# Optimization experiments

Hardware: AMD Instinct MI355X
Metric: run time of the kernel (lower is better)

The kernel has to match this reference:

```python
import jax, jax.numpy as jnp
import numpy as np

WIN = 5          # ssim_window_size
SIGMA = 1.5      # Gaussian sigma used by the reference implementation
C1 = 0.01 ** 2
C2 = 0.03 ** 2
MS_WEIGHTS = jnp.array([0.0448, 0.2856, 0.3001, 0.2363, 0.1333], dtype=jnp.float32)


def make_window(num_channel, dtype):
    x = jnp.arange(WIN, dtype=jnp.float32) - (WIN // 2)
    g = jnp.exp(-(x ** 2) / (2.0 * SIGMA ** 2))
    g = g / g.sum()
    w2 = jnp.outer(g, g)
    return jnp.broadcast_to(w2, (num_channel, 1, WIN, WIN)).astype(dtype)


def dwconv(x, w):
    pad = WIN // 2
    return jax.lax.conv_general_dilated(
        x, w, window_strides=(1, 1), padding=[(pad, pad), (pad, pad)],
        dimension_numbers=('NCHW', 'OIHW', 'NCHW'),
        feature_group_count=x.shape[1])


def compute_ssim(img1, img2):
    w = make_window(img1.shape[1], img1.dtype)
    mu1 = dwconv(img1, w)
    mu2 = dwconv(img2, w)
    mu1_sq = mu1 * mu1
    mu2_sq = mu2 * mu2
    mu1_mu2 = mu1 * mu2
    sigma1_sq = dwconv(img1 * img1, w) - mu1_sq
    sigma2_sq = dwconv(img2 * img2, w) - mu2_sq
    sigma12 = dwconv(img1 * img2, w) - mu1_mu2
    ssim_map = ((2 * mu1_mu2 + C1) * (2 * sigma12 + C2)) / (
        (mu1_sq + mu2_sq + C1) * (sigma1_sq + sigma2_sq + C2))
    cs = jnp.mean((2.0 * sigma12 + C2) / (sigma1_sq + sigma2_sq + C2))
    return jnp.mean(ssim_map), cs


def avg_pool2(x):
    s = jax.lax.reduce_window(x, jnp.array(0, x.dtype), jax.lax.add,
                              (1, 1, 2, 2), (1, 1, 2, 2), 'VALID')
    return s / jnp.array(4, x.dtype)


def ms_ssim(img1, img2):
    levels = MS_WEIGHTS.shape[0]
    ssims, mcs = [], []
    for _ in range(levels):
        s, cs = compute_ssim(img1, img2)
        ssims.append(s)
        mcs.append(cs)
        img1 = avg_pool2(img1)
        img2 = avg_pool2(img2)
    ssims = (jnp.stack(ssims) + 1) / 2
    mcs = (jnp.stack(mcs) + 1) / 2
    pow1 = mcs ** MS_WEIGHTS
    pow2 = ssims ** MS_WEIGHTS
    return jnp.prod(pow1[:-1] * pow2[-1])


def setup_inputs() -> dict:
    key = jax.random.key(0)
    k1, k2 = jax.random.split(key)
    shape = (32, 3, 512, 512)
    img1 = jax.random.uniform(k1, shape, dtype=jnp.float32)
    img2 = jax.random.uniform(k2, shape, dtype=jnp.float32)
    return {"img1": img1, "img2": img2}


def reference(img1, img2):
    return ms_ssim(img1, img2)
```

## Files before the change

### kernel.cpp

```cpp
#include <hip/hip_runtime.h>
#include <math.h>


typedef float f2 __attribute__((ext_vector_type(2)));

#if __has_builtin(__builtin_elementwise_fma)
static __device__ __forceinline__ f2 vfma(f2 a, f2 b, f2 c) {
    return __builtin_elementwise_fma(a, b, c);
}
#else
static __device__ __forceinline__ f2 vfma(f2 a, f2 b, f2 c) {
    f2 d; d.x = __builtin_fmaf(a.x, b.x, c.x); d.y = __builtin_fmaf(a.y, b.y, c.y);
    return d;
}
#endif

#define C1F 0.0001f
#define C2F 0.0009f
#define GW0f 0.12007838f
#define GW1f 0.23388060f
#define GW2f 0.29208204f

#define HCONV(DST, VL, V01, VR) do { \
    const f2 t1_ = (VL) + (VR); \
    f2 mid_; mid_.x = (VL).y + (V01).y; mid_.y = (V01).x + (VR).x; \
    (DST) = vfma(G1v, mid_, vfma(G0v, t1_, G2v * (V01))); \
} while (0)

#define VCONV(OUT, WN, S0,S1,S2,S3,S4) do { \
    const f2 t_ = WN[S0] + WN[S4]; \
    const f2 u_ = WN[S1] + WN[S3]; \
    (OUT) = vfma(G1v, u_, vfma(G0v, t_, G2v * WN[S2])); \
} while (0)

#define ROW(J,S0,S1,S2,S3,S4) do { \
    const int i = i0 + (J); \
    if (i < iters) { \
        const int r = y0 + i - 2; \
        f2 XL = {0.f,0.f}, X01 = {0.f,0.f}, XR = {0.f,0.f}; \
        f2 ZL = {0.f,0.f}, Z01 = {0.f,0.f}, ZR = {0.f,0.f}; \
        if ((unsigned)r < (unsigned)H) { \
            const float* r1_ = p1 + (size_t)r * (size_t)W; \
            const float* r2_ = p2 + (size_t)r * (size_t)W; \
            XL  = *(const f2*)(r1_ + offL) * mL; \
            X01 = *(const f2*)(r1_ + offC); \
            XR  = *(const f2*)(r1_ + offR) * mR; \
            ZL  = *(const f2*)(r2_ + offL) * mL; \
            Z01 = *(const f2*)(r2_ + offC); \
            ZR  = *(const f2*)(r2_ + offR) * mR; \
        } \
        const f2 QL = vfma(ZL,  ZL,  XL  * XL); \
        const f2 QC = vfma(Z01, Z01, X01 * X01); \
        const f2 QR = vfma(ZR,  ZR,  XR  * XR); \
        const f2 PL = XL  * ZL; \
        const f2 PC = X01 * Z01; \
        const f2 PR = XR  * ZR; \
        HCONV(wa[(J)], XL, X01, XR); \
        HCONV(wb[(J)], ZL, Z01, ZR); \
        HCONV(wq[(J)], QL, QC,  QR); \
        HCONV(wp[(J)], PL, PC,  PR); \
        if (i >= 4) { \
            f2 Av, Bv, Qv, Pv; \
            VCONV(Av, wa, S0,S1,S2,S3,S4); \
            VCONV(Bv, wb, S0,S1,S2,S3,S4); \
            VCONV(Qv, wq, S0,S1,S2,S3,S4); \
            VCONV(Pv, wp, S0,S1,S2,S3,S4); \
            const f2 ABv   = Av * Bv; \
            const f2 A2B2v = vfma(Bv, Bv, Av * Av); \
            const f2 S12v  = vfma(TWOv, Pv - ABv, C2v); \
            const f2 SDENv = (Qv - A2B2v) + C2v; \
            const f2 D1v   = A2B2v + C1v; \
            const f2 N1v   = vfma(TWOv, ABv, C1v); \
            const f2 DENv  = D1v * SDENv; \
            f2 RDv; \
            RDv.x = __builtin_amdgcn_rcpf(DENv.x); \
            RDv.y = __builtin_amdgcn_rcpf(DENv.y); \
            const f2 SSv = N1v * S12v * RDv; \
            const f2 CCv = S12v * D1v * RDv; \
            if (gC) { ACCS += SSv; ACCC += CCv; } \
        } \
        if (q1 && (i & 1) && i >= 3 && i <= TROWS + 1 && gC) { \
            const f2 sx_ = X01 + PX; \
            const f2 sz_ = Z01 + PZ; \
            const size_t po_ = (size_t)(r >> 1) * WP + (c0 >> 1); \
            q1[po_] = (sx_.x + sx_.y) * 0.25f; \
            q2[po_] = (sz_.x + sz_.y) * 0.25f; \
        } \
        PX = X01; PZ = Z01; \
    } \
} while (0)

template<int TROWS, int WPB>
__global__ __launch_bounds__(WPB * 64)
void ssim_level_kernel(const float* __restrict__ img1,
                       const float* __restrict__ img2,
                       int H, int W, int SX, int SY,
                       float* __restrict__ pool1,
                       float* __restrict__ pool2,
                       double* __restrict__ block_out)
{
    const int lane = threadIdx.x & 63;
    const int wv   = threadIdx.x >> 6;
    const int w    = blockIdx.x * WPB + wv;

    const int spp   = SX * SY;
    const int plane = w / spp;
    const int rem   = w - plane * spp;
    const int sy    = rem / SX;
    const int sx    = rem - sy * SX;

    const int base = sx * 128;
    const int y0   = sy * TROWS;
    const int c0   = base + 2 * lane;
    const bool gC = (unsigned)c0 < (unsigned)W;
    const bool gL = (c0 - 2) >= 0 && (c0 - 2) < W;
    const bool gR = (c0 + 2) < W;
    const int offL = gL ? (c0 - 2) : c0;
    const int offC = gC ? c0 : 0;
    const int offR = gR ? (c0 + 2) : 0;
    const f2 mL = {gL ? 1.f : 0.f, gL ? 1.f : 0.f};
    const f2 mR = {gR ? 1.f : 0.f, gR ? 1.f : 0.f};

    const float* p1 = img1 + (size_t)plane * H * W;
    const float* p2 = img2 + (size_t)plane * H * W;
    const int WP = W >> 1;
    float* q1 = pool1 ? pool1 + (size_t)plane * (H >> 1) * WP : nullptr;
    float* q2 = pool2 ? pool2 + (size_t)plane * (H >> 1) * WP : nullptr;

    const f2 G0v  = {GW0f, GW0f};
    const f2 G1v  = {GW1f, GW1f};
    const f2 G2v  = {GW2f, GW2f};
    const f2 C1v  = {C1F, C1F};
    const f2 C2v  = {C2F, C2F};
    const f2 TWOv = {2.f, 2.f};

    f2 wa[5], wb[5], wq[5], wp[5];
    f2 PX = {0.f, 0.f}, PZ = {0.f, 0.f};
    f2 ACCS = {0.f, 0.f}, ACCC = {0.f, 0.f};

    const int iters = TROWS + 4;
    for (int i0 = 0; i0 < iters; i0 += 5) {
        ROW(0, 1, 2, 3, 4, 0);
        ROW(1, 2, 3, 4, 0, 1);
        ROW(2, 3, 4, 0, 1, 2);
        ROW(3, 4, 0, 1, 2, 3);
        ROW(4, 0, 1, 2, 3, 4);
    }

    float accs = ACCS.x + ACCS.y;
    float accc = ACCC.x + ACCC.y;
    #pragma unroll
    for (int o = 32; o > 0; o >>= 1) {
        accs += __shfl_down(accs, o, 64);
        accc += __shfl_down(accc, o, 64);
    }

    __shared__ double sred[WPB][2];
    if (lane == 0) { sred[wv][0] = (double)accs; sred[wv][1] = (double)accc; }
    __syncthreads();
    if (threadIdx.x == 0) {
        double s = 0.0, c = 0.0;
        #pragma unroll
        for (int k = 0; k < WPB; ++k) { s += sred[k][0]; c += sred[k][1]; }
        block_out[2 * (size_t)blockIdx.x]     = s;
        block_out[2 * (size_t)blockIdx.x + 1] = c;
    }
}

static constexpr int NBLK[5] = {1536, 768, 384, 384, 192};
static constexpr int BOFF[5] = {0, 1536, 2304, 2688, 3072};

__global__ __launch_bounds__(1024)
void ssim_final_kernel(const double* __restrict__ bsum, float* __restrict__ out)
{
    __shared__ double partial[16][2];
    __shared__ double lvl[5][2];
    const double npx[5] = {96.0*512*512, 96.0*256*256, 96.0*128*128,
                           96.0*64*64,   96.0*32*32};
    const int tid = threadIdx.x, lane = tid & 63, wv = tid >> 6;

    for (int l = 0; l < 5; ++l) {
        double s = 0.0, c = 0.0;
        for (int k = tid; k < NBLK[l]; k += 1024) {
            s += bsum[2 * (size_t)(BOFF[l] + k)];
            c += bsum[2 * (size_t)(BOFF[l] + k) + 1];
        }
        #pragma unroll
        for (int o = 32; o > 0; o >>= 1) {
            s += __shfl_down(s, o, 64);
            c += __shfl_down(c, o, 64);
        }
        if (lane == 0) { partial[wv][0] = s; partial[wv][1] = c; }
        __syncthreads();
        if (tid == 0) {
            double ts = 0.0, tc = 0.0;
            for (int k = 0; k < 16; ++k) { ts += partial[k][0]; tc += partial[k][1]; }
            lvl[l][0] = ts / npx[l];
            lvl[l][1] = tc / npx[l];
        }
        __syncthreads();
    }
    if (tid == 0) {
        const double wgt[5] = {0.0448, 0.2856, 0.3001, 0.2363, 0.1333};
        double ssim4 = (lvl[4][0] + 1.0) * 0.5;
        double P = pow(ssim4, wgt[4]);
        double r = pow((lvl[0][1] + 1.0) * 0.5, wgt[0]) *
                   pow((lvl[1][1] + 1.0) * 0.5, wgt[1]) *
                   pow((lvl[2][1] + 1.0) * 0.5, wgt[2]) *
                   pow((lvl[3][1] + 1.0) * 0.5, wgt[3]);
        r *= P * P * P * P;
        out[0] = (float)r;
    }
}

extern "C" void kernel_launch(void* const* d_in, const int* in_sizes, int n_in,
                              void* d_out, int out_size, void* d_ws, size_t ws_size,
                              hipStream_t stream)
{
    const float* img1 = (const float*)d_in[0];
    const float* img2 = (const float*)d_in[1];
    float* out = (float*)d_out;

    char* ws = (char*)d_ws;
    double* wsum = (double*)ws;
    size_t off = 262144;
    const size_t P = 96;
    float* l1a = (float*)(ws + off); off += P * 256 * 256 * sizeof(float);
    float* l1b = (float*)(ws + off); off += P * 256 * 256 * sizeof(float);
    float* l2a = (float*)(ws + off); off += P * 128 * 128 * sizeof(float);
    float* l2b = (float*)(ws + off); off += P * 128 * 128 * sizeof(float);
    float* l3a = (float*)(ws + off); off += P * 64 * 64 * sizeof(float);
    float* l3b = (float*)(ws + off); off += P * 64 * 64 * sizeof(float);
    float* l4a = (float*)(ws + off); off += P * 32 * 32 * sizeof(float);
    float* l4b = (float*)(ws + off); off += P * 32 * 32 * sizeof(float);

    ssim_level_kernel<32, 4><<<1536, 256, 0, stream>>>(
        img1, img2, 512, 512, 4, 16, l1a, l1b, wsum + 2 * (size_t)BOFF[0]);
    ssim_level_kernel<16, 4><<<768, 256, 0, stream>>>(
        l1a, l1b, 256, 256, 2, 16, l2a, l2b, wsum + 2 * (size_t)BOFF[1]);
    ssim_level_kernel<8, 4><<<384, 256, 0, stream>>>(
        l2a, l2b, 128, 128, 1, 16, l3a, l3b, wsum + 2 * (size_t)BOFF[2]);
    ssim_level_kernel<4, 4><<<384, 256, 0, stream>>>(
        l3a, l3b, 64, 64, 1, 16, l4a, l4b, wsum + 2 * (size_t)BOFF[3]);
    ssim_level_kernel<4, 4><<<192, 256, 0, stream>>>(
        l4a, l4b, 32, 32, 1, 8, nullptr, nullptr, wsum + 2 * (size_t)BOFF[4]);

    ssim_final_kernel<<<1, 1024, 0, stream>>>(wsum, out);
}
```

Measured before the change: 300.8 us.

## Stage SSIM rows through LDS with async global_load_lds double buffering

Each level kernel now uses one wave per block that loads five-row batches of both images directly into LDS with global_load_lds, double-buffered with explicit vmcnt waits, then reads neighbors from LDS instead of issuing overlapping global loads. Column tiles overlap by halo (124 output columns per 128 loaded), tile heights and grids are retuned per level, and sizes are made compile-time template parameters. The per-block shared-memory reduction is dropped since each block is a single wave, at the cost of many more partial sums for the final kernel and redundant halo loads.

```diff
diff --git a/kernel.cpp b/kernel.cpp
--- a/kernel.cpp
+++ b/kernel.cpp
@@ -14,6 +14,18 @@
     return d;
 }
 #endif
+
+typedef __attribute__((address_space(1))) void gv_t;
+typedef __attribute__((address_space(3))) void lv_t;
+
+static __device__ __forceinline__ void gl_lds(const float* g, float* l) {
+    __builtin_amdgcn_global_load_lds((gv_t*)g, (lv_t*)l, 4, 0, 0);
+}
+
+#define WAITVM(N) do { \
+    asm volatile("s_waitcnt vmcnt(" #N ")" ::: "memory"); \
+    __builtin_amdgcn_sched_barrier(0); \
+} while (0)
 
 #define C1F 0.0001f
 #define C2F 0.0009f
@@ -33,97 +45,130 @@
     (OUT) = vfma(G1v, u_, vfma(G0v, t_, G2v * WN[S2])); \
 } while (0)
 
-#define ROW(J,S0,S1,S2,S3,S4) do { \
-    const int i = i0 + (J); \
-    if (i < iters) { \
-        const int r = y0 + i - 2; \
-        f2 XL = {0.f,0.f}, X01 = {0.f,0.f}, XR = {0.f,0.f}; \
-        f2 ZL = {0.f,0.f}, Z01 = {0.f,0.f}, ZR = {0.f,0.f}; \
-        if ((unsigned)r < (unsigned)H) { \
-            const float* r1_ = p1 + (size_t)r * (size_t)W; \
-            const float* r2_ = p2 + (size_t)r * (size_t)W; \
-            XL  = *(const f2*)(r1_ + offL) * mL; \
-            X01 = *(const f2*)(r1_ + offC); \
-            XR  = *(const f2*)(r1_ + offR) * mR; \
-            ZL  = *(const f2*)(r2_ + offL) * mL; \
-            Z01 = *(const f2*)(r2_ + offC); \
-            ZR  = *(const f2*)(r2_ + offR) * mR; \
-        } \
-        const f2 QL = vfma(ZL,  ZL,  XL  * XL); \
-        const f2 QC = vfma(Z01, Z01, X01 * X01); \
-        const f2 QR = vfma(ZR,  ZR,  XR  * XR); \
-        const f2 PL = XL  * ZL; \
-        const f2 PC = X01 * Z01; \
-        const f2 PR = XR  * ZR; \
-        HCONV(wa[(J)], XL, X01, XR); \
-        HCONV(wb[(J)], ZL, Z01, ZR); \
-        HCONV(wq[(J)], QL, QC,  QR); \
-        HCONV(wp[(J)], PL, PC,  PR); \
-        if (i >= 4) { \
-            f2 Av, Bv, Qv, Pv; \
-            VCONV(Av, wa, S0,S1,S2,S3,S4); \
-            VCONV(Bv, wb, S0,S1,S2,S3,S4); \
-            VCONV(Qv, wq, S0,S1,S2,S3,S4); \
-            VCONV(Pv, wp, S0,S1,S2,S3,S4); \
-            const f2 ABv   = Av * Bv; \
-            const f2 A2B2v = vfma(Bv, Bv, Av * Av); \
-            const f2 S12v  = vfma(TWOv, Pv - ABv, C2v); \
-            const f2 SDENv = (Qv - A2B2v) + C2v; \
-            const f2 D1v   = A2B2v + C1v; \
-            const f2 N1v   = vfma(TWOv, ABv, C1v); \
-            const f2 DENv  = D1v * SDENv; \
-            f2 RDv; \
-            RDv.x = __builtin_amdgcn_rcpf(DENv.x); \
-            RDv.y = __builtin_amdgcn_rcpf(DENv.y); \
-            const f2 SSv = N1v * S12v * RDv; \
-            const f2 CCv = S12v * D1v * RDv; \
-            if (gC) { ACCS += SSv; ACCC += CCv; } \
-        } \
-        if (q1 && (i & 1) && i >= 3 && i <= TROWS + 1 && gC) { \
+#define LOADB(T, B) do { \
+    _Pragma("unroll") \
+    for (int k_ = 0; k_ < 5; ++k_) { \
+        const int r_ = y0 + (T) * 5 + k_ - 2; \
+        const int rc_ = min(max(r_, 0), H - 1); \
+        const float* r1_ = p1 + (size_t)rc_ * W; \
+        const float* r2_ = p2 + (size_t)rc_ * W; \
+        gl_lds(r1_ + col1, &lds[B][k_][0][2]); \
+        gl_lds(r1_ + col2, &lds[B][k_][0][66]); \
+        gl_lds(r2_ + col1, &lds[B][k_][1][2]); \
+        gl_lds(r2_ + col2, &lds[B][k_][1][66]); \
+    } \
+} while (0)
+
+#define STEP(I, K, B, S0,S1,S2,S3,S4) do { \
+    const int r = y0 + (I) - 2; \
+    const float rv = ((unsigned)r < (unsigned)H) ? 1.f : 0.f; \
+    const f2 mVv = {rv, rv}; \
+    const f2 mLVv = mLv * mVv; \
+    const f2 mCVv = mCv * mVv; \
+    const f2 mRVv = mRv * mVv; \
+    const f2 XL  = *(const f2*)&lds[B][K][0][2 * lane]     * mLVv; \
+    const f2 X01 = *(const f2*)&lds[B][K][0][2 * lane + 2] * mCVv; \
+    const f2 XR  = *(const f2*)&lds[B][K][0][2 * lane + 4] * mRVv; \
+    const f2 ZL  = *(const f2*)&lds[B][K][1][2 * lane]     * mLVv; \
+    const f2 Z01 = *(const f2*)&lds[B][K][1][2 * lane + 2] * mCVv; \
+    const f2 ZR  = *(const f2*)&lds[B][K][1][2 * lane + 4] * mRVv; \
+    const f2 QL = vfma(ZL,  ZL,  XL  * XL); \
+    const f2 QC = vfma(Z01, Z01, X01 * X01); \
+    const f2 QR = vfma(ZR,  ZR,  XR  * XR); \
+    const f2 PL = XL  * ZL; \
+    const f2 PC = X01 * Z01; \
+    const f2 PR = XR  * ZR; \
+    HCONV(wa[(S4)], XL, X01, XR); \
+    HCONV(wb[(S4)], ZL, Z01, ZR); \
+    HCONV(wq[(S4)], QL, QC,  QR); \
+    HCONV(wp[(S4)], PL, PC,  PR); \
+    if ((I) >= 4) { \
+        f2 Av, Bv, Qv, Pv; \
+        VCONV(Av, wa, S0,S1,S2,S3,S4); \
+        VCONV(Bv, wb, S0,S1,S2,S3,S4); \
+        VCONV(Qv, wq, S0,S1,S2,S3,S4); \
+        VCONV(Pv, wp, S0,S1,S2,S3,S4); \
+        const f2 ABv   = Av * Bv; \
+        const f2 A2B2v = vfma(Bv, Bv, Av * Av); \
+        const f2 S12v  = vfma(TWOv, Pv - ABv, C2v); \
+        const f2 SDENv = (Qv - A2B2v) + C2v; \
+        const f2 D1v   = A2B2v + C1v; \
+        const f2 N1v   = vfma(TWOv, ABv, C1v); \
+        const f2 DENv  = D1v * SDENv; \
+        f2 RDv; \
+        RDv.x = __builtin_amdgcn_rcpf(DENv.x); \
+        RDv.y = __builtin_amdgcn_rcpf(DENv.y); \
+        const f2 SSv = N1v * S12v * RDv; \
+        const f2 CCv = S12v * D1v * RDv; \
+        ACCS += vout ? SSv : ZEROv; \
+        ACCC += vout ? CCv : ZEROv; \
+    } \
+    { \
+        const bool pcond = (TROWS == 1) ? ((I) == 2 && (y0 & 1)) \
+                          : (((I) & 1) && (I) >= 3 && (I) <= TROWS + 1); \
+        if (q1 && pcond && vout) { \
             const f2 sx_ = X01 + PX; \
             const f2 sz_ = Z01 + PZ; \
             const size_t po_ = (size_t)(r >> 1) * WP + (c0 >> 1); \
             q1[po_] = (sx_.x + sx_.y) * 0.25f; \
             q2[po_] = (sz_.x + sz_.y) * 0.25f; \
         } \
-        PX = X01; PZ = Z01; \
     } \
-} while (0)
-
-template<int TROWS, int WPB>
-__global__ __launch_bounds__(WPB * 64)
+    PX = X01; PZ = Z01; \
+} while (0)
+
+#define BATCH(T, B) do { \
+    STEP((T)*5+0, 0, B, 1,2,3,4,0); \
+    STEP((T)*5+1, 1, B, 2,3,4,0,1); \
+    STEP((T)*5+2, 2, B, 3,4,0,1,2); \
+    STEP((T)*5+3, 3, B, 4,0,1,2,3); \
+    STEP((T)*5+4, 4, B, 0,1,2,3,4); \
+} while (0)
+
+template<int TROWS, int H, int W, int SX>
+__global__ __launch_bounds__(64)
 void ssim_level_kernel(const float* __restrict__ img1,
                        const float* __restrict__ img2,
-                       int H, int W, int SX, int SY,
                        float* __restrict__ pool1,
                        float* __restrict__ pool2,
                        double* __restrict__ block_out)
 {
-    const int lane = threadIdx.x & 63;
-    const int wv   = threadIdx.x >> 6;
-    const int w    = blockIdx.x * WPB + wv;
-
-    const int spp   = SX * SY;
+    constexpr int SY = H / TROWS;
+    constexpr int spp = SX * SY;
+    constexpr int ITERS = TROWS + 4;
+    constexpr int NB = ITERS / 5;
+    static_assert(ITERS % 5 == 0, "TROWS+4 must be divisible by 5");
+    static_assert(NB == 1 || NB == 4, "pipeline written for NB in {1,4}");
+    constexpr int WP = W >> 1;
+
+    __shared__ float lds[2][5][2][132];
+
+    const int lane = threadIdx.x;
+    const int w    = blockIdx.x;
+
     const int plane = w / spp;
     const int rem   = w - plane * spp;
     const int sy    = rem / SX;
     const int sx    = rem - sy * SX;
 
-    const int base = sx * 128;
+    const int base = sx * 124;
     const int y0   = sy * TROWS;
-    const int c0   = base + 2 * lane;
-    const bool gC = (unsigned)c0 < (unsigned)W;
-    const bool gL = (c0 - 2) >= 0 && (c0 - 2) < W;
-    const bool gR = (c0 + 2) < W;
-    const int offL = gL ? (c0 - 2) : c0;
-    const int offC = gC ? c0 : 0;
-    const int offR = gR ? (c0 + 2) : 0;
-    const f2 mL = {gL ? 1.f : 0.f, gL ? 1.f : 0.f};
-    const f2 mR = {gR ? 1.f : 0.f, gR ? 1.f : 0.f};
-
-    const float* p1 = img1 + (size_t)plane * H * W;
-    const float* p2 = img2 + (size_t)plane * H * W;
-    const int WP = W >> 1;
+    const int c0   = base - 2 + 2 * lane;
+
+    const bool okL = (c0 >= 2) && (c0 <= W);
+    const bool okC = (c0 >= 0) && (c0 <= W - 2);
+    const bool okR = (c0 <= W - 4);
+    const bool vout = okC && lane >= 1 && lane <= 62;
+    const f2 mLv = {okL ? 1.f : 0.f, okL ? 1.f : 0.f};
+    const f2 mCv = {okC ? 1.f : 0.f, okC ? 1.f : 0.f};
+    const f2 mRv = {okR ? 1.f : 0.f, okR ? 1.f : 0.f};
+    const f2 ZEROv = {0.f, 0.f};
+
+    const int col1 = min(max(base - 2 + lane, 0), W - 1);
+    const int col2 = min(max(base + 62 + lane, 0), W - 1);
+
+    const float* p1 = img1 + (size_t)plane * (H * W);
+    const float* p2 = img2 + (size_t)plane * (H * W);
     float* q1 = pool1 ? pool1 + (size_t)plane * (H >> 1) * WP : nullptr;
     float* q2 = pool2 ? pool2 + (size_t)plane * (H >> 1) * WP : nullptr;
 
@@ -138,13 +183,23 @@
     f2 PX = {0.f, 0.f}, PZ = {0.f, 0.f};
     f2 ACCS = {0.f, 0.f}, ACCC = {0.f, 0.f};
 
-    const int iters = TROWS + 4;
-    for (int i0 = 0; i0 < iters; i0 += 5) {
-        ROW(0, 1, 2, 3, 4, 0);
-        ROW(1, 2, 3, 4, 0, 1);
-        ROW(2, 3, 4, 0, 1, 2);
-        ROW(3, 4, 0, 1, 2, 3);
-        ROW(4, 0, 1, 2, 3, 4);
+    if constexpr (NB == 4) {
+        LOADB(0, 0);
+        LOADB(1, 1);
+        WAITVM(20);
+        BATCH(0, 0);
+        LOADB(2, 0);
+        WAITVM(20);
+        BATCH(1, 1);
+        LOADB(3, 1);
+        WAITVM(20);
+        BATCH(2, 0);
+        WAITVM(0);
+        BATCH(3, 1);
+    } else {
+        LOADB(0, 0);
+        WAITVM(0);
+        BATCH(0, 0);
     }
 
     float accs = ACCS.x + ACCS.y;
@@ -154,21 +209,14 @@
         accs += __shfl_down(accs, o, 64);
         accc += __shfl_down(accc, o, 64);
     }
-
-    __shared__ double sred[WPB][2];
-    if (lane == 0) { sred[wv][0] = (double)accs; sred[wv][1] = (double)accc; }
-    __syncthreads();
-    if (threadIdx.x == 0) {
-        double s = 0.0, c = 0.0;
-        #pragma unroll
-        for (int k = 0; k < WPB; ++k) { s += sred[k][0]; c += sred[k][1]; }
-        block_out[2 * (size_t)blockIdx.x]     = s;
-        block_out[2 * (size_t)blockIdx.x + 1] = c;
-    }
-}
-
-static constexpr int NBLK[5] = {1536, 768, 384, 384, 192};
-static constexpr int BOFF[5] = {0, 1536, 2304, 2688, 3072};
+    if (lane == 0) {
+        block_out[2 * (size_t)w]     = (double)accs;
+        block_out[2 * (size_t)w + 1] = (double)accc;
+    }
+}
+
+static constexpr int NBLK[5] = {15360, 4608, 1536, 6144, 3072};
+static constexpr int BOFF[5] = {0, 15360, 19968, 21504, 27648};
 
 __global__ __launch_bounds__(1024)
 void ssim_final_kernel(const double* __restrict__ bsum, float* __restrict__ out)
@@ -223,7 +271,7 @@
 
     char* ws = (char*)d_ws;
     double* wsum = (double*)ws;
-    size_t off = 262144;
+    size_t off = 524288;
     const size_t P = 96;
     float* l1a = (float*)(ws + off); off += P * 256 * 256 * sizeof(float);
     float* l1b = (float*)(ws + off); off += P * 256 * 256 * sizeof(float);
@@ -234,16 +282,16 @@
     float* l4a = (float*)(ws + off); off += P * 32 * 32 * sizeof(float);
     float* l4b = (float*)(ws + off); off += P * 32 * 32 * sizeof(float);
 
-    ssim_level_kernel<32, 4><<<1536, 256, 0, stream>>>(
-        img1, img2, 512, 512, 4, 16, l1a, l1b, wsum + 2 * (size_t)BOFF[0]);
-    ssim_level_kernel<16, 4><<<768, 256, 0, stream>>>(
-        l1a, l1b, 256, 256, 2, 16, l2a, l2b, wsum + 2 * (size_t)BOFF[1]);
-    ssim_level_kernel<8, 4><<<384, 256, 0, stream>>>(
-        l2a, l2b, 128, 128, 1, 16, l3a, l3b, wsum + 2 * (size_t)BOFF[2]);
-    ssim_level_kernel<4, 4><<<384, 256, 0, stream>>>(
-        l3a, l3b, 64, 64, 1, 16, l4a, l4b, wsum + 2 * (size_t)BOFF[3]);
-    ssim_level_kernel<4, 4><<<192, 256, 0, stream>>>(
-        l4a, l4b, 32, 32, 1, 8, nullptr, nullptr, wsum + 2 * (size_t)BOFF[4]);
+    ssim_level_kernel<16, 512, 512, 5><<<15360, 64, 0, stream>>>(
+        img1, img2, l1a, l1b, wsum + 2 * (size_t)BOFF[0]);
+    ssim_level_kernel<16, 256, 256, 3><<<4608, 64, 0, stream>>>(
+        l1a, l1b, l2a, l2b, wsum + 2 * (size_t)BOFF[1]);
+    ssim_level_kernel<16, 128, 128, 2><<<1536, 64, 0, stream>>>(
+        l2a, l2b, l3a, l3b, wsum + 2 * (size_t)BOFF[2]);
+    ssim_level_kernel<1, 64, 64, 1><<<6144, 64, 0, stream>>>(
+        l3a, l3b, l4a, l4b, wsum + 2 * (size_t)BOFF[3]);
+    ssim_level_kernel<1, 32, 32, 1><<<3072, 64, 0, stream>>>(
+        l4a, l4b, nullptr, nullptr, wsum + 2 * (size_t)BOFF[4]);
 
     ssim_final_kernel<<<1, 1024, 0, stream>>>(wsum, out);
 }
```

New measurement: 305.4 us. No clear change (+1.5%).
